# Performance work log

Measured on AMD Instinct MI355X. Metric: run time of the kernel, lower is better.

Reference implementation:

```python
import jax, jax.numpy as jnp
import numpy as np

# Multi-scale feature pyramid (H, W) per level: strides 8/16/32/64 on a ~512px image
SHAPES = ((64, 64), (32, 32), (16, 16), (8, 8))
N_HEADS, N_LEVELS, N_POINTS = 8, 4, 4
D_MODEL = 256
HEAD_DIM = D_MODEL // N_HEADS


def setup_inputs() -> dict:
    key = jax.random.key(0)
    ks = jax.random.split(key, 11)
    B, C = 4, D_MODEL
    Lv = sum(h * w for h, w in SHAPES)  # 5440
    Lq = Lv  # encoder self-attention: queries are the flattened features
    scale = 0.02
    return {
        "query": jax.random.normal(ks[0], (B, Lq, C), jnp.float32),
        "reference_points": jax.random.uniform(ks[1], (B, Lq, N_LEVELS, 2), jnp.float32),
        "value": jax.random.normal(ks[2], (B, Lv, C), jnp.float32),
        "W_off": jax.random.normal(ks[3], (C, N_HEADS * N_LEVELS * N_POINTS * 2), jnp.float32) * scale,
        "b_off": jax.random.normal(ks[4], (N_HEADS * N_LEVELS * N_POINTS * 2,), jnp.float32) * 0.5,
        "W_attn": jax.random.normal(ks[5], (C, N_HEADS * N_LEVELS * N_POINTS), jnp.float32) * scale,
        "b_attn": jax.random.normal(ks[6], (N_HEADS * N_LEVELS * N_POINTS,), jnp.float32) * scale,
        "W_val": jax.random.normal(ks[7], (C, C), jnp.float32) * scale,
        "b_val": jax.random.normal(ks[8], (C,), jnp.float32) * scale,
        "W_out": jax.random.normal(ks[9], (C, C), jnp.float32) * scale,
        "b_out": jax.random.normal(ks[10], (C,), jnp.float32) * scale,
    }


def _bilinear_sample(val, grid, H, W):
    """Replicates F.grid_sample(mode='bilinear', padding_mode='zeros', align_corners=False).

    val:  [N, C, H, W]
    grid: [N, Lq, P, 2] in [-1, 1] (x, y order)
    returns: [N, C, Lq, P]
    """
    N, C = val.shape[0], val.shape[1]
    # unnormalize (align_corners=False)
    x = (grid[..., 0] + 1.0) * 0.5 * W - 0.5  # [N, Lq, P]
    y = (grid[..., 1] + 1.0) * 0.5 * H - 0.5
    x0 = jnp.floor(x)
    y0 = jnp.floor(y)
    wx = x - x0  # fractional parts
    wy = y - y0
    flat = val.reshape(N, C, H * W)

    def gather(xi, yi):
        valid = (xi >= 0) & (xi < W) & (yi >= 0) & (yi < H)
        xc = jnp.clip(xi, 0, W - 1).astype(jnp.int32)
        yc = jnp.clip(yi, 0, H - 1).astype(jnp.int32)
        idx = yc * W + xc  # [N, Lq, P]
        g = jax.vmap(lambda v, i: v[:, i])(flat, idx)  # [N, C, Lq, P]
        return g * valid[:, None, :, :].astype(val.dtype)

    out = (gather(x0, y0) * ((1 - wx) * (1 - wy))[:, None]
           + gather(x0 + 1, y0) * (wx * (1 - wy))[:, None]
           + gather(x0, y0 + 1) * ((1 - wx) * wy)[:, None]
           + gather(x0 + 1, y0 + 1) * (wx * wy)[:, None])
    return out


def _ms_deform_attn(query, reference_points, value, W_off, b_off, W_attn, b_attn,
                    W_val, b_val, W_out, b_out):
    B, Lq, C = query.shape
    val = value @ W_val + b_val  # [B, Lv, C]
    val = val.reshape(B, -1, N_HEADS, HEAD_DIM)

    offsets = (query @ W_off + b_off).reshape(B, Lq, N_HEADS, N_LEVELS, N_POINTS, 2)
    weights = jax.nn.softmax(
        (query @ W_attn + b_attn).reshape(B, Lq, N_HEADS, N_LEVELS * N_POINTS), axis=-1
    ).reshape(B, Lq, N_HEADS, N_LEVELS, N_POINTS)

    # offset normalizer: (W, H) per level
    offset_norm = jnp.array([[w, h] for h, w in SHAPES], jnp.float32)
    # ref_dim == 2 branch
    locs = reference_points[:, :, None, :, None, :] + offsets / offset_norm[None, None, None, :, None, :]
    grids = 2.0 * locs - 1.0  # [B, Lq, nh, nl, np, 2]

    acc = jnp.zeros((B * N_HEADS, HEAD_DIM, Lq), query.dtype)
    start = 0
    for lid, (H, W) in enumerate(SHAPES):
        # [B, HW, nh, hd] -> [B*nh, hd, H, W]
        v = val[:, start:start + H * W].transpose(0, 2, 3, 1).reshape(B * N_HEADS, HEAD_DIM, H, W)
        g = grids[:, :, :, lid].transpose(0, 2, 1, 3, 4).reshape(B * N_HEADS, Lq, N_POINTS, 2)
        s = _bilinear_sample(v, g, H, W)  # [B*nh, hd, Lq, np]
        w = weights[:, :, :, lid].transpose(0, 2, 1, 3).reshape(B * N_HEADS, 1, Lq, N_POINTS)
        acc = acc + (s * w).sum(-1)
        start += H * W

    out = acc.reshape(B, D_MODEL, Lq).transpose(0, 2, 1)  # [B, Lq, C]
    return out @ W_out + b_out


def reference(query, reference_points, value, W_off, b_off, W_attn, b_attn,
              W_val, b_val, W_out, b_out):
    return _ms_deform_attn(query, reference_points, value, W_off, b_off,
                           W_attn, b_attn, W_val, b_val, W_out, b_out)
```

## Files before the change

kernel.cpp:

```cpp
#include <hip/hip_runtime.h>


typedef __attribute__((ext_vector_type(8))) _Float16 half8;
typedef __attribute__((ext_vector_type(4))) float f32x4;

typedef __attribute__((address_space(3))) unsigned int lds_uint;
typedef const __attribute__((address_space(1))) unsigned int g_uint;

__device__ __forceinline__ void load_lds16(const _Float16* g, _Float16* l) {
    __builtin_amdgcn_global_load_lds((g_uint*)g, (lds_uint*)l, 16, 0, 0);
}

__device__ __forceinline__ half8 splat8(_Float16 v) {
    half8 r = {v, v, v, v, v, v, v, v};
    return r;
}

#define M_TOTAL 21760

__global__ __launch_bounds__(256) void gemm12_cvt(
    const float* __restrict__ value, const float* __restrict__ query,
    const float* __restrict__ W_val, const float* __restrict__ W_off,
    const float* __restrict__ W_attn,
    const float* __restrict__ b_val, const float* __restrict__ b_off,
    const float* __restrict__ b_attn,
    _Float16* __restrict__ valh, _Float16* __restrict__ offh)
{
    __shared__ _Float16 As[128 * 34];
    __shared__ _Float16 Bs[64 * 34];

    const bool g1 = blockIdx.x < 680;
    const int id = g1 ? blockIdx.x : blockIdx.x - 680;
    const int mt = g1 ? (id >> 2) : (id / 6);
    const int nt = g1 ? (id & 3) : (id % 6);
    const int NN = g1 ? 256 : 384;
    const float* A = g1 ? value : query;
    _Float16* C = g1 ? valh : offh;
    const int bm = mt * 128;
    const int bn = nt * 64;

    const float* W;
    int sW, nb;
    if (g1)           { W = W_val;  sW = 256; nb = bn; }
    else if (bn < 256){ W = W_off;  sW = 256; nb = bn; }
    else              { W = W_attn; sW = 128; nb = bn - 256; }

    const int tid = threadIdx.x;
    const int wave = tid >> 6, lane = tid & 63;
    const int wm = (wave & 1) * 64, wn = (wave >> 1) * 32;
    const int ml = lane & 15, kq = (lane >> 4) * 8;

    const int ar = tid >> 1, akb = (tid & 1) * 16;
    const int bn_l = tid & 63, bk8 = (tid >> 6) * 8;

    const f32x4 zero4 = {0.f, 0.f, 0.f, 0.f};
    f32x4 acc[4][2];
#pragma unroll
    for (int i = 0; i < 4; ++i)
#pragma unroll
        for (int j = 0; j < 2; ++j) acc[i][j] = zero4;

    for (int kt = 0; kt < 8; ++kt) {
        const int k0 = kt * 32;
        const float* as = A + (size_t)(bm + ar) * 256 + k0 + akb;
        const float4 a0 = *(const float4*)(as + 0);
        const float4 a1 = *(const float4*)(as + 4);
        const float4 a2 = *(const float4*)(as + 8);
        const float4 a3 = *(const float4*)(as + 12);
        float bv[8];
#pragma unroll
        for (int j = 0; j < 8; ++j)
            bv[j] = W[(size_t)(k0 + bk8 + j) * sW + nb + bn_l];

        const half8 ha0 = {(_Float16)a0.x, (_Float16)a0.y, (_Float16)a0.z, (_Float16)a0.w,
                           (_Float16)a1.x, (_Float16)a1.y, (_Float16)a1.z, (_Float16)a1.w};
        const half8 ha1 = {(_Float16)a2.x, (_Float16)a2.y, (_Float16)a2.z, (_Float16)a2.w,
                           (_Float16)a3.x, (_Float16)a3.y, (_Float16)a3.z, (_Float16)a3.w};
        const half8 hb = {(_Float16)bv[0], (_Float16)bv[1], (_Float16)bv[2], (_Float16)bv[3],
                          (_Float16)bv[4], (_Float16)bv[5], (_Float16)bv[6], (_Float16)bv[7]};

        __syncthreads();
        *(half8*)(As + ar * 34 + akb) = ha0;
        *(half8*)(As + ar * 34 + akb + 8) = ha1;
        *(half8*)(Bs + bn_l * 34 + bk8) = hb;
        __syncthreads();

        half8 af[4], bf[2];
#pragma unroll
        for (int i = 0; i < 4; ++i)
            af[i] = *(const half8*)(As + (wm + i * 16 + ml) * 34 + kq);
#pragma unroll
        for (int j = 0; j < 2; ++j)
            bf[j] = *(const half8*)(Bs + (wn + j * 16 + ml) * 34 + kq);
#pragma unroll
        for (int i = 0; i < 4; ++i)
#pragma unroll
            for (int j = 0; j < 2; ++j)
                acc[i][j] = __builtin_amdgcn_mfma_f32_16x16x32_f16(af[i], bf[j], acc[i][j], 0, 0, 0);
    }

    const int r0 = (lane >> 4) * 4;
#pragma unroll
    for (int j = 0; j < 2; ++j) {
        const int col = bn + wn + j * 16 + ml;
        const float bj = g1 ? b_val[col] : (col < 256 ? b_off[col] : b_attn[col - 256]);
#pragma unroll
        for (int i = 0; i < 4; ++i) {
            const size_t rbase = (size_t)(bm + wm + i * 16 + r0) * NN + col;
#pragma unroll
            for (int r = 0; r < 4; ++r)
                C[rbase + (size_t)r * NN] = (_Float16)(acc[i][j][r] + bj);
        }
    }
}

__device__ __forceinline__ void gemm_core(
    const _Float16* __restrict__ A, const _Float16* __restrict__ Bt,
    const float* __restrict__ bias, float* __restrict__ Cv,
    int NN, int mt, int nt)
{
    __shared__ _Float16 Ah[128 * 32];
    __shared__ _Float16 Bh[64 * 32];

    const int tid = threadIdx.x;
    const int bm = mt * 128;
    const int bn = nt * 64;
    const int wave = tid >> 6, lane = tid & 63;
    const int wm = (wave & 1) * 64, wn = (wave >> 1) * 32;
    const int ml = lane & 15, kq = (lane >> 4) * 8;
    const int lr = lane >> 2;
    const int lk = (lane & 3) * 8;

    const f32x4 zero4 = {0.f, 0.f, 0.f, 0.f};
    f32x4 acc[4][2];
#pragma unroll
    for (int i = 0; i < 4; ++i)
#pragma unroll
        for (int j = 0; j < 2; ++j) acc[i][j] = zero4;

    for (int kt = 0; kt < 8; ++kt) {
        const int k0 = kt * 32;
        __syncthreads();
#pragma unroll
        for (int t = 0; t < 2; ++t) {
            const int row = wave * 32 + t * 16;
            load_lds16(A + (size_t)(bm + row + lr) * 256 + k0 + lk,
                       Ah + (size_t)row * 32);
        }
        {
            const int row = wave * 16;
            load_lds16(Bt + (size_t)(bn + row + lr) * 256 + k0 + lk,
                       Bh + (size_t)row * 32);
        }
        __syncthreads();

        half8 af[4], bf[2];
#pragma unroll
        for (int i = 0; i < 4; ++i)
            af[i] = *(const half8*)(Ah + (wm + i * 16 + ml) * 32 + kq);
#pragma unroll
        for (int j = 0; j < 2; ++j)
            bf[j] = *(const half8*)(Bh + (wn + j * 16 + ml) * 32 + kq);
#pragma unroll
        for (int i = 0; i < 4; ++i)
#pragma unroll
            for (int j = 0; j < 2; ++j)
                acc[i][j] = __builtin_amdgcn_mfma_f32_16x16x32_f16(af[i], bf[j], acc[i][j], 0, 0, 0);
    }

    const int r0 = (lane >> 4) * 4;
#pragma unroll
    for (int j = 0; j < 2; ++j) {
        const int col = bn + wn + j * 16 + ml;
        const float bj = bias[col];
#pragma unroll
        for (int i = 0; i < 4; ++i) {
            const size_t rbase = (size_t)(bm + wm + i * 16 + r0) * NN + col;
#pragma unroll
            for (int r = 0; r < 4; ++r)
                Cv[rbase + (size_t)r * NN] = acc[i][j][r] + bj;
        }
    }
}

__global__ __launch_bounds__(256) void gemm_single(
    const _Float16* __restrict__ A, const _Float16* __restrict__ Bt,
    const float* __restrict__ bias, float* __restrict__ Cv)
{
    const int id = blockIdx.x;
    gemm_core(A, Bt, bias, Cv, 256, id >> 2, id & 3);
}

__global__ __launch_bounds__(256) void sample_f16(
    const _Float16* __restrict__ valh,
    const float* __restrict__ refp,
    const _Float16* __restrict__ offh,
    const float* __restrict__ W_out,
    _Float16* __restrict__ wto,
    _Float16* __restrict__ acc_out)
{
    if (blockIdx.x < 256)
        wto[blockIdx.x * 256 + threadIdx.x] =
            (_Float16)W_out[threadIdx.x * 256 + blockIdx.x];

    const int wave = threadIdx.x >> 6, lane = threadIdx.x & 63;
    const int q2 = lane >> 5, sl = lane & 31;
    const int bq = blockIdx.x * 8 + wave * 2 + q2;
    const int b = bq / 5440;
    const int h = sl >> 2;
    const int d8 = (sl & 3) * 8;

    const _Float16* off_row = offh + (size_t)bq * 384 + h * 32;
    const _Float16* att_row = offh + (size_t)bq * 384 + 256 + h * 16;
    const float* rp = refp + (size_t)bq * 8;

    float offv[32];
#pragma unroll
    for (int i = 0; i < 4; ++i) {
        const half8 t = *(const half8*)(off_row + i * 8);
#pragma unroll
        for (int j = 0; j < 8; ++j) offv[i * 8 + j] = (float)t[j];
    }
    float lg[16];
    {
        const half8 t0 = *(const half8*)(att_row);
        const half8 t1 = *(const half8*)(att_row + 8);
#pragma unroll
        for (int j = 0; j < 8; ++j) { lg[j] = (float)t0[j]; lg[8 + j] = (float)t1[j]; }
    }
    float mx = -1e30f;
#pragma unroll
    for (int i = 0; i < 16; ++i) mx = fmaxf(mx, lg[i]);
    float s = 0.f;
#pragma unroll
    for (int i = 0; i < 16; ++i) { lg[i] = __expf(lg[i] - mx); s += lg[i]; }
    const float inv = 1.f / s;

    const float4 rp01 = *(const float4*)rp;
    const float4 rp23 = *(const float4*)(rp + 4);
    const float rxs[4] = {rp01.x, rp01.z, rp23.x, rp23.z};
    const float rys[4] = {rp01.y, rp01.w, rp23.y, rp23.w};

    const int Ws_[4] = {64, 32, 16, 8};
    const int starts_[4] = {0, 4096, 5120, 5376};

    half8 acc = splat8((_Float16)0.f);
#pragma unroll
    for (int l = 0; l < 4; ++l) {
        const int W = Ws_[l];
        const float fW = (float)W;
        const _Float16* vbase = valh + ((size_t)(b * 5440 + starts_[l])) * 256 + h * 32 + d8;
        const float rx = rxs[l], ry = rys[l];
#pragma unroll
        for (int p = 0; p < 4; ++p) {
            const int pi = l * 4 + p;
            const float aw = lg[pi] * inv;
            const float x = fmaf(rx, fW, offv[pi * 2 + 0]) - 0.5f;
            const float y = fmaf(ry, fW, offv[pi * 2 + 1]) - 0.5f;
            const float x0f = floorf(x), y0f = floorf(y);
            const int x0 = (int)x0f, y0 = (int)y0f;
            const float wx = x - x0f, wy = y - y0f;
            const bool okx0 = ((unsigned)x0 < (unsigned)W);
            const bool okx1 = ((unsigned)(x0 + 1) < (unsigned)W);
            const bool oky0 = ((unsigned)y0 < (unsigned)W);
            const bool oky1 = ((unsigned)(y0 + 1) < (unsigned)W);
            const int xc0 = min(max(x0, 0), W - 1);
            const int xc1 = min(max(x0 + 1, 0), W - 1);
            const int yc0 = min(max(y0, 0), W - 1);
            const int yc1 = min(max(y0 + 1, 0), W - 1);
            const float w00 = (okx0 & oky0) ? (1.f - wx) * (1.f - wy) * aw : 0.f;
            const float w10 = (okx1 & oky0) ? wx * (1.f - wy) * aw : 0.f;
            const float w01 = (okx0 & oky1) ? (1.f - wx) * wy * aw : 0.f;
            const float w11 = (okx1 & oky1) ? wx * wy * aw : 0.f;

            const half8 c00 = *(const half8*)(vbase + (size_t)(yc0 * W + xc0) * 256);
            const half8 c10 = *(const half8*)(vbase + (size_t)(yc0 * W + xc1) * 256);
            const half8 c01 = *(const half8*)(vbase + (size_t)(yc1 * W + xc0) * 256);
            const half8 c11 = *(const half8*)(vbase + (size_t)(yc1 * W + xc1) * 256);

            acc += c00 * splat8((_Float16)w00);
            acc += c10 * splat8((_Float16)w10);
            acc += c01 * splat8((_Float16)w01);
            acc += c11 * splat8((_Float16)w11);
        }
    }

    *(half8*)(acc_out + (size_t)bq * 256 + h * 32 + d8) = acc;
}

extern "C" void kernel_launch(void* const* d_in, const int* in_sizes, int n_in,
                              void* d_out, int out_size, void* d_ws, size_t ws_size,
                              hipStream_t stream) {
    const float* query  = (const float*)d_in[0];
    const float* refp   = (const float*)d_in[1];
    const float* value  = (const float*)d_in[2];
    const float* W_off  = (const float*)d_in[3];
    const float* b_off  = (const float*)d_in[4];
    const float* W_attn = (const float*)d_in[5];
    const float* b_attn = (const float*)d_in[6];
    const float* W_val  = (const float*)d_in[7];
    const float* b_val  = (const float*)d_in[8];
    const float* W_out  = (const float*)d_in[9];
    const float* b_out  = (const float*)d_in[10];
    float* out = (float*)d_out;

    const size_t M = M_TOTAL;

    _Float16* valh  = (_Float16*)d_ws;
    _Float16* offh  = valh + M * 256;
    _Float16* acc16 = offh + M * 384;
    _Float16* wto   = acc16 + M * 256;

    dim3 blk(256);
    gemm12_cvt<<<dim3(1700), blk, 0, stream>>>(
        value, query, W_val, W_off, W_attn, b_val, b_off, b_attn, valh, offh);
    sample_f16<<<dim3(M / 8), blk, 0, stream>>>(valh, refp, offh, W_out, wto, acc16);
    gemm_single<<<dim3(680), blk, 0, stream>>>(acc16, wto, b_out, out);
}
```

Baseline: 187.7 us.

## Widen fused projection GEMM tile to 128 and batch gathers per level

The first GEMM now uses a 128x128 output tile per block instead of 128x64, which halves the block count and reuses each A tile across more columns, so the fp32 activation reads and conversions are repeated less often. The sampling kernel computes all 16 bilinear indices and weights for a level first, then issues the 16 gathers together before accumulating, so more loads are in flight at once. It also keeps the offsets as packed halves and adds a launch-bounds occupancy hint of 4 blocks. The costs are more registers per thread and fewer blocks in the GEMM.

```diff
diff --git a/kernel.cpp b/kernel.cpp
--- a/kernel.cpp
+++ b/kernel.cpp
@@ -27,38 +27,38 @@
     _Float16* __restrict__ valh, _Float16* __restrict__ offh)
 {
     __shared__ _Float16 As[128 * 34];
-    __shared__ _Float16 Bs[64 * 34];
-
-    const bool g1 = blockIdx.x < 680;
-    const int id = g1 ? blockIdx.x : blockIdx.x - 680;
-    const int mt = g1 ? (id >> 2) : (id / 6);
-    const int nt = g1 ? (id & 3) : (id % 6);
+    __shared__ _Float16 Bs[128 * 34];
+
+    const bool g1 = blockIdx.x < 340;
+    const int id = g1 ? blockIdx.x : blockIdx.x - 340;
+    const int mt = g1 ? (id >> 1) : (id / 3);
+    const int nt = g1 ? (id & 1) : (id % 3);
     const int NN = g1 ? 256 : 384;
     const float* A = g1 ? value : query;
     _Float16* C = g1 ? valh : offh;
     const int bm = mt * 128;
-    const int bn = nt * 64;
+    const int bn = nt * 128;
 
     const float* W;
     int sW, nb;
-    if (g1)           { W = W_val;  sW = 256; nb = bn; }
-    else if (bn < 256){ W = W_off;  sW = 256; nb = bn; }
-    else              { W = W_attn; sW = 128; nb = bn - 256; }
+    if (g1)            { W = W_val;  sW = 256; nb = bn; }
+    else if (nt < 2)   { W = W_off;  sW = 256; nb = bn; }
+    else               { W = W_attn; sW = 128; nb = 0;  }
 
     const int tid = threadIdx.x;
     const int wave = tid >> 6, lane = tid & 63;
-    const int wm = (wave & 1) * 64, wn = (wave >> 1) * 32;
+    const int wm = (wave & 1) * 64, wn = (wave >> 1) * 64;
     const int ml = lane & 15, kq = (lane >> 4) * 8;
 
     const int ar = tid >> 1, akb = (tid & 1) * 16;
-    const int bn_l = tid & 63, bk8 = (tid >> 6) * 8;
+    const int bn_l = tid & 127, bkg = (tid >> 7) * 16;
 
     const f32x4 zero4 = {0.f, 0.f, 0.f, 0.f};
-    f32x4 acc[4][2];
+    f32x4 acc[4][4];
 #pragma unroll
     for (int i = 0; i < 4; ++i)
 #pragma unroll
-        for (int j = 0; j < 2; ++j) acc[i][j] = zero4;
+        for (int j = 0; j < 4; ++j) acc[i][j] = zero4;
 
     for (int kt = 0; kt < 8; ++kt) {
         const int k0 = kt * 32;
@@ -67,41 +67,44 @@
         const float4 a1 = *(const float4*)(as + 4);
         const float4 a2 = *(const float4*)(as + 8);
         const float4 a3 = *(const float4*)(as + 12);
-        float bv[8];
-#pragma unroll
-        for (int j = 0; j < 8; ++j)
-            bv[j] = W[(size_t)(k0 + bk8 + j) * sW + nb + bn_l];
+        float bv[16];
+#pragma unroll
+        for (int j = 0; j < 16; ++j)
+            bv[j] = W[(size_t)(k0 + bkg + j) * sW + nb + bn_l];
 
         const half8 ha0 = {(_Float16)a0.x, (_Float16)a0.y, (_Float16)a0.z, (_Float16)a0.w,
                            (_Float16)a1.x, (_Float16)a1.y, (_Float16)a1.z, (_Float16)a1.w};
         const half8 ha1 = {(_Float16)a2.x, (_Float16)a2.y, (_Float16)a2.z, (_Float16)a2.w,
                            (_Float16)a3.x, (_Float16)a3.y, (_Float16)a3.z, (_Float16)a3.w};
-        const half8 hb = {(_Float16)bv[0], (_Float16)bv[1], (_Float16)bv[2], (_Float16)bv[3],
-                          (_Float16)bv[4], (_Float16)bv[5], (_Float16)bv[6], (_Float16)bv[7]};
+        const half8 hb0 = {(_Float16)bv[0], (_Float16)bv[1], (_Float16)bv[2], (_Float16)bv[3],
+                           (_Float16)bv[4], (_Float16)bv[5], (_Float16)bv[6], (_Float16)bv[7]};
+        const half8 hb1 = {(_Float16)bv[8], (_Float16)bv[9], (_Float16)bv[10], (_Float16)bv[11],
+                           (_Float16)bv[12], (_Float16)bv[13], (_Float16)bv[14], (_Float16)bv[15]};
 
         __syncthreads();
         *(half8*)(As + ar * 34 + akb) = ha0;
         *(half8*)(As + ar * 34 + akb + 8) = ha1;
-        *(half8*)(Bs + bn_l * 34 + bk8) = hb;
+        *(half8*)(Bs + bn_l * 34 + bkg) = hb0;
+        *(half8*)(Bs + bn_l * 34 + bkg + 8) = hb1;
         __syncthreads();
 
-        half8 af[4], bf[2];
+        half8 af[4], bf[4];
 #pragma unroll
         for (int i = 0; i < 4; ++i)
             af[i] = *(const half8*)(As + (wm + i * 16 + ml) * 34 + kq);
 #pragma unroll
-        for (int j = 0; j < 2; ++j)
+        for (int j = 0; j < 4; ++j)
             bf[j] = *(const half8*)(Bs + (wn + j * 16 + ml) * 34 + kq);
 #pragma unroll
         for (int i = 0; i < 4; ++i)
 #pragma unroll
-            for (int j = 0; j < 2; ++j)
+            for (int j = 0; j < 4; ++j)
                 acc[i][j] = __builtin_amdgcn_mfma_f32_16x16x32_f16(af[i], bf[j], acc[i][j], 0, 0, 0);
     }
 
     const int r0 = (lane >> 4) * 4;
 #pragma unroll
-    for (int j = 0; j < 2; ++j) {
+    for (int j = 0; j < 4; ++j) {
         const int col = bn + wn + j * 16 + ml;
         const float bj = g1 ? b_val[col] : (col < 256 ? b_off[col] : b_attn[col - 256]);
 #pragma unroll
@@ -191,7 +194,7 @@
     gemm_core(A, Bt, bias, Cv, 256, id >> 2, id & 3);
 }
 
-__global__ __launch_bounds__(256) void sample_f16(
+__global__ __launch_bounds__(256, 4) void sample_f16(
     const _Float16* __restrict__ valh,
     const float* __restrict__ refp,
     const _Float16* __restrict__ offh,
@@ -214,13 +217,10 @@
     const _Float16* att_row = offh + (size_t)bq * 384 + 256 + h * 16;
     const float* rp = refp + (size_t)bq * 8;
 
-    float offv[32];
-#pragma unroll
-    for (int i = 0; i < 4; ++i) {
-        const half8 t = *(const half8*)(off_row + i * 8);
-#pragma unroll
-        for (int j = 0; j < 8; ++j) offv[i * 8 + j] = (float)t[j];
-    }
+    const half8 ofr0 = *(const half8*)(off_row);
+    const half8 ofr1 = *(const half8*)(off_row + 8);
+    const half8 ofr2 = *(const half8*)(off_row + 16);
+    const half8 ofr3 = *(const half8*)(off_row + 24);
     float lg[16];
     {
         const half8 t0 = *(const half8*)(att_row);
@@ -251,12 +251,23 @@
         const float fW = (float)W;
         const _Float16* vbase = valh + ((size_t)(b * 5440 + starts_[l])) * 256 + h * 32 + d8;
         const float rx = rxs[l], ry = rys[l];
+
+        int idx_[16];
+        _Float16 w_[16];
 #pragma unroll
         for (int p = 0; p < 4; ++p) {
             const int pi = l * 4 + p;
             const float aw = lg[pi] * inv;
-            const float x = fmaf(rx, fW, offv[pi * 2 + 0]) - 0.5f;
-            const float y = fmaf(ry, fW, offv[pi * 2 + 1]) - 0.5f;
+            float ox, oy;
+            {
+                const half8 src = (pi < 8) ? ((pi < 4) ? ofr0 : ofr1)
+                                           : ((pi < 12) ? ofr2 : ofr3);
+                const int e = (pi & 3) * 2;
+                ox = (float)src[e];
+                oy = (float)src[e + 1];
+            }
+            const float x = fmaf(rx, fW, ox) - 0.5f;
+            const float y = fmaf(ry, fW, oy) - 0.5f;
             const float x0f = floorf(x), y0f = floorf(y);
             const int x0 = (int)x0f, y0 = (int)y0f;
             const float wx = x - x0f, wy = y - y0f;
@@ -268,21 +279,23 @@
             const int xc1 = min(max(x0 + 1, 0), W - 1);
             const int yc0 = min(max(y0, 0), W - 1);
             const int yc1 = min(max(y0 + 1, 0), W - 1);
-            const float w00 = (okx0 & oky0) ? (1.f - wx) * (1.f - wy) * aw : 0.f;
-            const float w10 = (okx1 & oky0) ? wx * (1.f - wy) * aw : 0.f;
-            const float w01 = (okx0 & oky1) ? (1.f - wx) * wy * aw : 0.f;
-            const float w11 = (okx1 & oky1) ? wx * wy * aw : 0.f;
-
-            const half8 c00 = *(const half8*)(vbase + (size_t)(yc0 * W + xc0) * 256);
-            const half8 c10 = *(const half8*)(vbase + (size_t)(yc0 * W + xc1) * 256);
-            const half8 c01 = *(const half8*)(vbase + (size_t)(yc1 * W + xc0) * 256);
-            const half8 c11 = *(const half8*)(vbase + (size_t)(yc1 * W + xc1) * 256);
-
-            acc += c00 * splat8((_Float16)w00);
-            acc += c10 * splat8((_Float16)w10);
-            acc += c01 * splat8((_Float16)w01);
-            acc += c11 * splat8((_Float16)w11);
-        }
+            w_[p * 4 + 0] = (_Float16)((okx0 & oky0) ? (1.f - wx) * (1.f - wy) * aw : 0.f);
+            w_[p * 4 + 1] = (_Float16)((okx1 & oky0) ? wx * (1.f - wy) * aw : 0.f);
+            w_[p * 4 + 2] = (_Float16)((okx0 & oky1) ? (1.f - wx) * wy * aw : 0.f);
+            w_[p * 4 + 3] = (_Float16)((okx1 & oky1) ? wx * wy * aw : 0.f);
+            idx_[p * 4 + 0] = (yc0 * W + xc0) * 256;
+            idx_[p * 4 + 1] = (yc0 * W + xc1) * 256;
+            idx_[p * 4 + 2] = (yc1 * W + xc0) * 256;
+            idx_[p * 4 + 3] = (yc1 * W + xc1) * 256;
+        }
+
+        half8 c_[16];
+#pragma unroll
+        for (int i = 0; i < 16; ++i)
+            c_[i] = *(const half8*)(vbase + idx_[i]);
+#pragma unroll
+        for (int i = 0; i < 16; ++i)
+            acc += c_[i] * splat8(w_[i]);
     }
 
     *(half8*)(acc_out + (size_t)bq * 256 + h * 32 + d8) = acc;
@@ -312,7 +325,7 @@
     _Float16* wto   = acc16 + M * 256;
 
     dim3 blk(256);
-    gemm12_cvt<<<dim3(1700), blk, 0, stream>>>(
+    gemm12_cvt<<<dim3(850), blk, 0, stream>>>(
         value, query, W_val, W_off, W_attn, b_val, b_off, b_attn, valh, offh);
     sample_f16<<<dim3(M / 8), blk, 0, stream>>>(valh, refp, offh, W_out, wto, acc16);
     gemm_single<<<dim3(680), blk, 0, stream>>>(acc16, wto, b_out, out);
```

Measured after the change: 180.1 us. 1.04x faster.
